# Kernel tuning notes

Hardware: AMD Instinct MI355X
Metric: run time of the kernel (lower is better)

## Reference

```python
import jax, jax.numpy as jnp
from jax import lax
import numpy as np

EPS = 1e-6
B, CIN, HW = 16, 12, 40
E, DEPTH, NH = 768, 12, 12
K, PAD = 10, 5
S = (HW + 2 * PAD - K) // 1 + 1  # 41 (series_len = s0); s1 also 41
L = S * S
HD = E // NH
MLP = 4 * E


def _ln(x, w, b):
    mu = x.mean(-1, keepdims=True)
    xc = x - mu
    var = (xc * xc).mean(-1, keepdims=True)
    return xc * lax.rsqrt(var + EPS) * w + b


def setup_inputs() -> dict:
    key = jax.random.key(0)
    ks = iter(jax.random.split(key, 24))
    r = lambda shape, s=0.02: jax.random.normal(next(ks), shape, jnp.float32) * s
    inp = {
        'x': jax.random.normal(next(ks), (B, CIN, HW, HW), jnp.float32),
        'conv_w': r((E, CIN, K, K)), 'conv_b': jnp.zeros((E,), jnp.float32),
        'pos_embed': r((1, L, E)),
        'ln1_w': jnp.ones((DEPTH, E), jnp.float32), 'ln1_b': jnp.zeros((DEPTH, E), jnp.float32),
        'qkv_w': r((DEPTH, E, 3 * E)), 'qkv_b': jnp.zeros((DEPTH, 3 * E), jnp.float32),
        'proj_w': r((DEPTH, E, E)), 'proj_b': jnp.zeros((DEPTH, E), jnp.float32),
        'ln2_w': jnp.ones((DEPTH, E), jnp.float32), 'ln2_b': jnp.zeros((DEPTH, E), jnp.float32),
        'fc1_w': r((DEPTH, E, MLP)), 'fc1_b': jnp.zeros((DEPTH, MLP), jnp.float32),
        'fc2_w': r((DEPTH, MLP, E)), 'fc2_b': jnp.zeros((DEPTH, E), jnp.float32),
        'lnf_w': jnp.ones((E,), jnp.float32), 'lnf_b': jnp.zeros((E,), jnp.float32),
        'tconv_w': r((E, 1, K, K)), 'tconv_b': jnp.zeros((1,), jnp.float32),
    }
    return inp


def reference(x, conv_w, conv_b, pos_embed, ln1_w, ln1_b, qkv_w, qkv_b,
              proj_w, proj_b, ln2_w, ln2_b, fc1_w, fc1_b, fc2_w, fc2_b,
              lnf_w, lnf_b, tconv_w, tconv_b):
    scale = HD ** -0.5
    # patch embed: Conv2d -> (B, E, 41, 41) -> flatten -> (B, L, E)
    h = lax.conv_general_dilated(x, conv_w, (1, 1), [(PAD, PAD), (PAD, PAD)])
    h = h + conv_b[None, :, None, None]
    t = h.reshape(B, E, L).transpose(0, 2, 1) + pos_embed

    for i in range(DEPTH):
        # attention over each of the S series slices (N = S tokens each), batched
        y = _ln(t, ln1_w[i], ln1_b[i])
        qkv = (y @ qkv_w[i] + qkv_b[i]).reshape(B, S, S, 3, NH, HD)
        q, k, v = qkv[:, :, :, 0], qkv[:, :, :, 1], qkv[:, :, :, 2]  # (B,S,N,NH,HD)
        attn = jnp.einsum('bsnhd,bsmhd->bshnm', q, k) * scale
        attn = jax.nn.softmax(attn, axis=-1)
        o = jnp.einsum('bshnm,bsmhd->bsnhd', attn, v).reshape(B, L, E)
        t = t + (o @ proj_w[i] + proj_b[i])
        # MLP
        z = _ln(t, ln2_w[i], ln2_b[i])
        z = jax.nn.gelu(z @ fc1_w[i] + fc1_b[i], approximate=False)
        t = t + (z @ fc2_w[i] + fc2_b[i])

    t = _ln(t, lnf_w, lnf_b)
    feat = t.reshape(B, S, S, E).transpose(0, 3, 1, 2)  # (B, E, 41, 41)
    # ConvTranspose2d(k=10, s=1, p=5) == direct conv with flipped/swapped kernel, pad k-1-p=4
    wt = jnp.flip(tconv_w, (2, 3)).transpose(1, 0, 2, 3)  # (out_c, E, K, K)
    out = lax.conv_general_dilated(feat, wt, (1, 1), [(K - 1 - PAD,) * 2] * 2)
    out = out + tconv_b[None, :, None, None]
    return jnp.squeeze(out)  # (B, 40, 40)
```

## Files before the change

kernel.cpp:

```cpp
#include <hip/hip_runtime.h>
#include <cstdint>

typedef __bf16 bf16_t;
typedef __attribute__((ext_vector_type(8))) __bf16 bf16x8;
typedef __attribute__((ext_vector_type(4))) __bf16 bf16x4;
typedef __attribute__((ext_vector_type(4))) float f32x4;

#define TOKENS 26896
#define LLEN   1681
#define SDIM   41
#define EDIM   768

__device__ __forceinline__ void gload_lds16(const bf16_t* g, bf16_t* l) {
  auto gp = reinterpret_cast<const __attribute__((address_space(1))) char*>(
      reinterpret_cast<uintptr_t>(g));
  auto lp = reinterpret_cast<__attribute__((address_space(3))) char*>(
      reinterpret_cast<uintptr_t>(l));
  __builtin_amdgcn_global_load_lds(gp, lp, 16, 0, 0);
}

enum { EPI_T_POS = 0, EPI_BF16 = 1, EPI_ADD_T = 2, EPI_GELU = 3, EPI_F32 = 4 };

template <int EPI>
__global__ __launch_bounds__(256, 4) void gemm4_kernel(
    const bf16_t* __restrict__ A, const bf16_t* __restrict__ Bt,
    const float* __restrict__ bias, float* __restrict__ fout,
    bf16_t* __restrict__ bout, const float* __restrict__ pos,
    int M, int N, int K, int ntn, int nwg)
{
  __shared__ bf16_t lds[16384];
  const int tid = threadIdx.x, wave = tid >> 6, lane = tid & 63;
  const int wr = wave >> 1, wc = wave & 1;

  int id = blockIdx.x;
  {
    const int q = nwg >> 3, r = nwg & 7;
    const int xcd = id & 7, ix = id >> 3;
    id = (xcd < r ? xcd * (q + 1) : r * (q + 1) + (xcd - r) * q) + ix;
  }
  const int row0 = (id / ntn) * 128;
  const int col0 = (id % ntn) * 128;
  const int NT = K >> 5;

  const int srow = tid >> 2;
  const int sswz = ((tid & 3) ^ ((srow >> 1) & 3)) * 8;
  const bf16_t* aptr[2];
  const bf16_t* bptr[2];
  #pragma unroll
  for (int p = 0; p < 2; ++p) {
    int ar = row0 + p * 64 + srow; if (ar > M - 1) ar = M - 1;
    int br = col0 + p * 64 + srow; if (br > N - 1) br = N - 1;
    aptr[p] = A  + (size_t)ar * K + sswz;
    bptr[p] = Bt + (size_t)br * K + sswz;
  }
  bf16_t* sdst = lds + tid * 8;

  #define STAGE(BUF, KT) do {                                   \
    const int koff_ = (KT) << 5;                                \
    gload_lds16(aptr[0] + koff_, sdst + (BUF)*8192);            \
    gload_lds16(aptr[1] + koff_, sdst + (BUF)*8192 + 2048);     \
    gload_lds16(bptr[0] + koff_, sdst + (BUF)*8192 + 4096);     \
    gload_lds16(bptr[1] + koff_, sdst + (BUF)*8192 + 6144);     \
  } while (0)

  const int l15 = lane & 15, l4 = lane >> 4;
  const int fswz = (l4 ^ ((l15 >> 1) & 3)) << 3;
  const bf16_t* lA = lds + (wr * 64 + l15) * 32 + fswz;
  const bf16_t* lB = lds + 4096 + (wc * 64 + l15) * 32 + fswz;

  f32x4 acc[4][4] = {};

  #define COMPUTE(BUF) do {                                     \
    bf16x8 fa[4], fb[4];                                        \
    _Pragma("unroll")                                           \
    for (int m_ = 0; m_ < 4; ++m_) fa[m_] = *(const bf16x8*)(lA + (BUF)*8192 + m_*512); \
    _Pragma("unroll")                                           \
    for (int n_ = 0; n_ < 4; ++n_) fb[n_] = *(const bf16x8*)(lB + (BUF)*8192 + n_*512); \
    _Pragma("unroll")                                           \
    for (int m_ = 0; m_ < 4; ++m_)                              \
      _Pragma("unroll")                                         \
      for (int n_ = 0; n_ < 4; ++n_)                            \
        acc[m_][n_] = __builtin_amdgcn_mfma_f32_16x16x32_bf16(fa[m_], fb[n_], acc[m_][n_], 0, 0, 0); \
  } while (0)

  STAGE(0, 0);
  __syncthreads();
  int kt = 0;
  while (kt + 2 <= NT) {
    if (kt + 1 < NT) STAGE(1, kt + 1);
    COMPUTE(0);
    __syncthreads();
    if (kt + 2 < NT) STAGE(0, kt + 2);
    COMPUTE(1);
    __syncthreads();
    kt += 2;
  }
  if (kt < NT) COMPUTE(0);
  #undef STAGE
  #undef COMPUTE

  const int rgrp = lane >> 4;
  #pragma unroll
  for (int m = 0; m < 4; ++m) {
    #pragma unroll
    for (int n = 0; n < 4; ++n) {
      const int col = col0 + wc * 64 + n * 16 + l15;
      if (col >= N) continue;
      const int rbase = row0 + wr * 64 + m * 16 + rgrp * 4;
      float bv = 0.f;
      if constexpr (EPI != EPI_F32) bv = bias[col];
      #pragma unroll
      for (int r = 0; r < 4; ++r) {
        const int rr = rbase + r;
        if (rr >= M) continue;
        const float v = acc[m][n][r] + bv;
        const size_t o = (size_t)rr * N + col;
        if constexpr (EPI == EPI_T_POS) {
          const int l = rr % LLEN;
          fout[o] = v + pos[(size_t)l * N + col];
        } else if constexpr (EPI == EPI_BF16) {
          bout[o] = (bf16_t)v;
        } else if constexpr (EPI == EPI_ADD_T) {
          fout[o] += v;
        } else if constexpr (EPI == EPI_GELU) {
          const float gg = 0.5f * v * (1.f + erff(v * 0.70710678118654752f));
          bout[o] = (bf16_t)gg;
        } else {
          fout[o] = v;
        }
      }
    }
  }
}

__global__ __launch_bounds__(256) void gemm128_f32(
    const bf16_t* __restrict__ A, const bf16_t* __restrict__ Bt,
    float* __restrict__ fout, int M, int N, int K)
{
  __shared__ bf16_t As[128 * 32];
  __shared__ bf16_t Bs[128 * 32];
  const int tid = threadIdx.x, wave = tid >> 6, lane = tid & 63;
  const int row0 = blockIdx.x * 128, col0 = blockIdx.y * 128;
  const int wr = wave >> 1, wc = wave & 1;
  f32x4 acc[4][4] = {};
  const int srow = lane >> 2, skoff = (lane & 3) * 8;
  const int nsteps = K >> 5;
  for (int kt = 0; kt < nsteps; ++kt) {
    const int k0 = kt << 5;
    #pragma unroll
    for (int i = 0; i < 2; ++i) {
      const int r = (i * 4 + wave) * 16 + srow;
      int arow = row0 + r; if (arow > M - 1) arow = M - 1;
      int brow = col0 + r; if (brow > N - 1) brow = N - 1;
      gload_lds16(A  + (size_t)arow * K + k0 + skoff, &As[r * 32 + skoff]);
      gload_lds16(Bt + (size_t)brow * K + k0 + skoff, &Bs[r * 32 + skoff]);
    }
    asm volatile("s_waitcnt vmcnt(0)" ::: "memory");
    __syncthreads();
    const int lrow = lane & 15, lk = (lane >> 4) * 8;
    bf16x8 af[4], bfr[4];
    #pragma unroll
    for (int mi = 0; mi < 4; ++mi)
      af[mi] = *(const bf16x8*)&As[(wr * 64 + mi * 16 + lrow) * 32 + lk];
    #pragma unroll
    for (int ni = 0; ni < 4; ++ni)
      bfr[ni] = *(const bf16x8*)&Bs[(wc * 64 + ni * 16 + lrow) * 32 + lk];
    #pragma unroll
    for (int mi = 0; mi < 4; ++mi)
      #pragma unroll
      for (int ni = 0; ni < 4; ++ni)
        acc[mi][ni] = __builtin_amdgcn_mfma_f32_16x16x32_bf16(af[mi], bfr[ni], acc[mi][ni], 0, 0, 0);
    __syncthreads();
  }
  const int lcol = lane & 15, rgrp = lane >> 4;
  #pragma unroll
  for (int mi = 0; mi < 4; ++mi)
    #pragma unroll
    for (int ni = 0; ni < 4; ++ni) {
      const int col = col0 + wc * 64 + ni * 16 + lcol;
      if (col >= N) continue;
      const int rbase = row0 + wr * 64 + mi * 16 + rgrp * 4;
      #pragma unroll
      for (int r = 0; r < 4; ++r) {
        const int rr = rbase + r;
        if (rr >= M) continue;
        fout[(size_t)rr * N + col] = acc[mi][ni][r];
      }
    }
}

__global__ __launch_bounds__(256) void ln_kernel(
    const float* __restrict__ t, const float* __restrict__ w,
    const float* __restrict__ b, bf16_t* __restrict__ y)
{
  const int token = blockIdx.x * 4 + (threadIdx.x >> 6);
  const int lane  = threadIdx.x & 63;
  const float4* xp = (const float4*)(t + (size_t)token * EDIM);
  float4 v[3];
  float s = 0.f;
  #pragma unroll
  for (int i = 0; i < 3; ++i) {
    v[i] = xp[i * 64 + lane];
    s += v[i].x + v[i].y + v[i].z + v[i].w;
  }
  #pragma unroll
  for (int off = 32; off; off >>= 1) s += __shfl_xor(s, off);
  const float mu = s * (1.f / 768.f);
  float q = 0.f;
  #pragma unroll
  for (int i = 0; i < 3; ++i) {
    const float dx = v[i].x - mu, dy = v[i].y - mu;
    const float dz = v[i].z - mu, dw = v[i].w - mu;
    q += dx * dx + dy * dy + dz * dz + dw * dw;
  }
  #pragma unroll
  for (int off = 32; off; off >>= 1) q += __shfl_xor(q, off);
  const float rs = rsqrtf(q * (1.f / 768.f) + 1e-6f);
  bf16_t* yp = y + (size_t)token * EDIM;
  #pragma unroll
  for (int i = 0; i < 3; ++i) {
    const int e = i * 64 + lane;
    const float4 wv = ((const float4*)w)[e];
    const float4 bv = ((const float4*)b)[e];
    bf16x4 o;
    o[0] = (bf16_t)((v[i].x - mu) * rs * wv.x + bv.x);
    o[1] = (bf16_t)((v[i].y - mu) * rs * wv.y + bv.y);
    o[2] = (bf16_t)((v[i].z - mu) * rs * wv.z + bv.z);
    o[3] = (bf16_t)((v[i].w - mu) * rs * wv.w + bv.w);
    *(bf16x4*)(yp + e * 4) = o;
  }
}

__global__ __launch_bounds__(256) void attn_kernel(
    const bf16_t* __restrict__ qkv, bf16_t* __restrict__ o)
{
  const int blk = blockIdx.x;
  const int h  = blk % 12;
  const int bs = blk / 12;
  const int s1 = bs % SDIM;
  const int b  = bs / SDIM;
  __shared__ float Qs[SDIM][65], Ks[SDIM][65], Vs[SDIM][65], Ps[SDIM][44];
  const int tid = threadIdx.x;
  const size_t base = ((size_t)b * LLEN + (size_t)s1 * SDIM);

  for (int idx = tid; idx < SDIM * 8; idx += 256) {
    const int m = idx >> 3, c = idx & 7;
    const bf16_t* p = qkv + (base + m) * 2304 + h * 64 + c * 8;
    const bf16x8 qv = *(const bf16x8*)(p);
    const bf16x8 kv = *(const bf16x8*)(p + 768);
    const bf16x8 vv = *(const bf16x8*)(p + 1536);
    #pragma unroll
    for (int j = 0; j < 8; ++j) {
      Qs[m][c * 8 + j] = (float)qv[j];
      Ks[m][c * 8 + j] = (float)kv[j];
      Vs[m][c * 8 + j] = (float)vv[j];
    }
  }
  __syncthreads();

  for (int idx = tid; idx < SDIM * SDIM; idx += 256) {
    const int n = idx / SDIM, m = idx % SDIM;
    float s = 0.f;
    #pragma unroll
    for (int d = 0; d < 64; ++d) s += Qs[n][d] * Ks[m][d];
    Ps[n][m] = s * 0.125f;
  }
  __syncthreads();

  {
    const int row = tid >> 2, sub = tid & 3;
    if (row < SDIM) {
      float mx = -1e30f;
      for (int m = sub; m < SDIM; m += 4) mx = fmaxf(mx, Ps[row][m]);
      mx = fmaxf(mx, __shfl_xor(mx, 1));
      mx = fmaxf(mx, __shfl_xor(mx, 2));
      float sum = 0.f;
      for (int m = sub; m < SDIM; m += 4) {
        const float e = __expf(Ps[row][m] - mx);
        Ps[row][m] = e;
        sum += e;
      }
      sum += __shfl_xor(sum, 1);
      sum += __shfl_xor(sum, 2);
      const float inv = 1.f / sum;
      for (int m = sub; m < SDIM; m += 4) Ps[row][m] *= inv;
    }
  }
  __syncthreads();

  for (int idx = tid; idx < SDIM * 64; idx += 256) {
    const int n = idx >> 6, d = idx & 63;
    float s = 0.f;
    #pragma unroll
    for (int m = 0; m < SDIM; ++m) s += Ps[n][m] * Vs[m][d];
    o[(base + n) * EDIM + h * 64 + d] = (bf16_t)s;
  }
}

__global__ __launch_bounds__(256) void transpose_kernel(
    const float* __restrict__ in, bf16_t* __restrict__ out, int K, int N)
{
  __shared__ float tile[32][33];
  const int k0 = blockIdx.x * 32, n0 = blockIdx.y * 32;
  const int tx = threadIdx.x & 31, ty = threadIdx.x >> 5;
  #pragma unroll
  for (int i = 0; i < 32; i += 8) {
    const int k = k0 + ty + i, n = n0 + tx;
    if (k < K && n < N) tile[ty + i][tx] = in[(size_t)k * N + n];
  }
  __syncthreads();
  #pragma unroll
  for (int i = 0; i < 32; i += 8) {
    const int n = n0 + ty + i, k = k0 + tx;
    if (n < N && k < K) out[(size_t)n * K + k] = (bf16_t)tile[tx][ty + i];
  }
}

__global__ __launch_bounds__(256) void im2col_kernel(
    const float* __restrict__ x, bf16_t* __restrict__ col, int tok0, int ntok)
{
  const size_t idx = (size_t)blockIdx.x * 256 + threadIdx.x;
  if (idx >= (size_t)ntok * 1216) return;
  const int kk = (int)(idx % 1216);
  const size_t tok = tok0 + idx / 1216;
  const int b = (int)(tok / LLEN), l = (int)(tok % LLEN);
  const int s1 = l / SDIM, s2 = l % SDIM;
  float v = 0.f;
  if (kk < 1200) {
    const int cin = kk / 100, r = kk % 100, ky = r / 10, kx = r % 10;
    const int iy = s1 - 5 + ky, ix = s2 - 5 + kx;
    if (iy >= 0 && iy < 40 && ix >= 0 && ix < 40)
      v = x[((size_t)(b * 12 + cin) * 40 + iy) * 40 + ix];
  }
  col[idx] = (bf16_t)v;
}

__global__ __launch_bounds__(256) void convw_kernel(
    const float* __restrict__ w, bf16_t* __restrict__ out)
{
  const int idx = blockIdx.x * 256 + threadIdx.x;
  const int kk = idx % 1216, e = idx / 1216;
  const float v = (kk < 1200) ? w[(size_t)e * 1200 + kk] : 0.f;
  out[idx] = (bf16_t)v;
}

__global__ __launch_bounds__(256) void tconvw_kernel(
    const float* __restrict__ w, bf16_t* __restrict__ out)
{
  const int idx = blockIdx.x * 256 + threadIdx.x;
  const int e = idx % 768, tap = idx / 768;
  const int ky = tap / 10, kx = tap % 10;
  out[idx] = (bf16_t)w[(size_t)e * 100 + (9 - ky) * 10 + (9 - kx)];
}

__global__ __launch_bounds__(256) void outconv_kernel(
    const float* __restrict__ g, const float* __restrict__ tb,
    float* __restrict__ out)
{
  const int idx = blockIdx.x * 256 + threadIdx.x;
  if (idx >= 16 * 40 * 40) return;
  const int x = idx % 40, y = (idx / 40) % 40, b = idx / 1600;
  float s = tb[0];
  #pragma unroll
  for (int ky = 0; ky < 10; ++ky) {
    const int ty_ = y - 4 + ky;
    if (ty_ < 0 || ty_ >= SDIM) continue;
    #pragma unroll
    for (int kx = 0; kx < 10; ++kx) {
      const int tx_ = x - 4 + kx;
      if (tx_ < 0 || tx_ >= SDIM) continue;
      s += g[((size_t)b * LLEN + ty_ * SDIM + tx_) * 100 + ky * 10 + kx];
    }
  }
  out[idx] = s;
}

extern "C" void kernel_launch(void* const* d_in, const int* in_sizes, int n_in,
                              void* d_out, int out_size, void* d_ws, size_t ws_size,
                              hipStream_t stream)
{
  const float* x       = (const float*)d_in[0];
  const float* conv_w  = (const float*)d_in[1];
  const float* conv_b  = (const float*)d_in[2];
  const float* pos     = (const float*)d_in[3];
  const float* ln1_w   = (const float*)d_in[4];
  const float* ln1_b   = (const float*)d_in[5];
  const float* qkv_w   = (const float*)d_in[6];
  const float* qkv_b   = (const float*)d_in[7];
  const float* proj_w  = (const float*)d_in[8];
  const float* proj_b  = (const float*)d_in[9];
  const float* ln2_w   = (const float*)d_in[10];
  const float* ln2_b   = (const float*)d_in[11];
  const float* fc1_w   = (const float*)d_in[12];
  const float* fc1_b   = (const float*)d_in[13];
  const float* fc2_w   = (const float*)d_in[14];
  const float* fc2_b   = (const float*)d_in[15];
  const float* lnf_w   = (const float*)d_in[16];
  const float* lnf_b   = (const float*)d_in[17];
  const float* tconv_w = (const float*)d_in[18];
  const float* tconv_b = (const float*)d_in[19];
  float* out = (float*)d_out;

  const int nch = (ws_size >= 303500000UL) ? 1
                : (ws_size >= 220900000UL) ? 2 : 4;
  const int cht = TOKENS / nch;

  char* p = (char*)d_ws;
  auto alloc = [&](size_t bytes) {
    char* r = p;
    p += (bytes + 255) & ~(size_t)255;
    return r;
  };
  bf16_t* wbuf = (bf16_t*)alloc((size_t)768 * 9216 * 2);
  float*  t    = (float*)alloc((size_t)TOKENS * EDIM * 4);
  bf16_t* ybuf = (bf16_t*)alloc((size_t)TOKENS * EDIM * 2);
  bf16_t* hbuf = (bf16_t*)alloc((size_t)cht * 3072 * 2);

  bf16_t* Wq = wbuf;
  bf16_t* Wp = Wq + (size_t)2304 * 768;
  bf16_t* W1 = Wp + (size_t)768 * 768;
  bf16_t* W2 = W1 + (size_t)3072 * 768;

  auto g4 = [&](int epi, const bf16_t* A, const bf16_t* Bt,
                const float* bias, float* fo, bf16_t* bo, const float* pe,
                int M, int N, int K) {
    const int mtiles = (M + 127) / 128;
    const int ntn = N / 128;
    const int nwg = mtiles * ntn;
    switch (epi) {
      case EPI_T_POS: gemm4_kernel<EPI_T_POS><<<nwg, 256, 0, stream>>>(A, Bt, bias, fo, bo, pe, M, N, K, ntn, nwg); break;
      case EPI_BF16:  gemm4_kernel<EPI_BF16 ><<<nwg, 256, 0, stream>>>(A, Bt, bias, fo, bo, pe, M, N, K, ntn, nwg); break;
      case EPI_ADD_T: gemm4_kernel<EPI_ADD_T><<<nwg, 256, 0, stream>>>(A, Bt, bias, fo, bo, pe, M, N, K, ntn, nwg); break;
      default:        gemm4_kernel<EPI_GELU ><<<nwg, 256, 0, stream>>>(A, Bt, bias, fo, bo, pe, M, N, K, ntn, nwg); break;
    }
  };

  convw_kernel<<<(768 * 1216) / 256, 256, 0, stream>>>(conv_w, wbuf);
  for (int c = 0; c < nch; ++c) {
    const int tok0 = c * cht;
    im2col_kernel<<<(unsigned)(((size_t)cht * 1216 + 255) / 256), 256, 0, stream>>>(x, hbuf, tok0, cht);
    g4(EPI_T_POS, hbuf, wbuf, conv_b, t + (size_t)tok0 * EDIM, nullptr, pos, cht, EDIM, 1216);
  }

  for (int i = 0; i < 12; ++i) {
    transpose_kernel<<<dim3(24, 72), 256, 0, stream>>>(qkv_w + (size_t)i * 768 * 2304, Wq, 768, 2304);
    transpose_kernel<<<dim3(24, 24), 256, 0, stream>>>(proj_w + (size_t)i * 768 * 768, Wp, 768, 768);
    transpose_kernel<<<dim3(24, 96), 256, 0, stream>>>(fc1_w + (size_t)i * 768 * 3072, W1, 768, 3072);
    transpose_kernel<<<dim3(96, 24), 256, 0, stream>>>(fc2_w + (size_t)i * 3072 * 768, W2, 3072, 768);

    ln_kernel<<<TOKENS / 4, 256, 0, stream>>>(t, ln1_w + i * EDIM, ln1_b + i * EDIM, ybuf);
    for (int c = 0; c < nch; ++c) {
      const size_t ro = (size_t)c * cht;
      g4(EPI_BF16, ybuf + ro * EDIM, Wq, qkv_b + i * 2304, nullptr, hbuf, nullptr, cht, 2304, 768);
      attn_kernel<<<(16 / nch) * SDIM * 12, 256, 0, stream>>>(hbuf, ybuf + ro * EDIM);
    }
    g4(EPI_ADD_T, ybuf, Wp, proj_b + i * EDIM, t, nullptr, nullptr, TOKENS, EDIM, 768);

    ln_kernel<<<TOKENS / 4, 256, 0, stream>>>(t, ln2_w + i * EDIM, ln2_b + i * EDIM, ybuf);
    for (int c = 0; c < nch; ++c) {
      const size_t ro = (size_t)c * cht;
      g4(EPI_GELU, ybuf + ro * EDIM, W1, fc1_b + i * 3072, nullptr, hbuf, nullptr, cht, 3072, 768);
      g4(EPI_ADD_T, hbuf, W2, fc2_b + i * EDIM, t + ro * EDIM, nullptr, nullptr, cht, EDIM, 3072);
    }
  }

  ln_kernel<<<TOKENS / 4, 256, 0, stream>>>(t, lnf_w, lnf_b, ybuf);
  tconvw_kernel<<<(100 * 768) / 256, 256, 0, stream>>>(tconv_w, wbuf);
  gemm128_f32<<<dim3((TOKENS + 127) / 128, 1), 256, 0, stream>>>(ybuf, wbuf, (float*)hbuf, TOKENS, 100, 768);
  outconv_kernel<<<100, 256, 0, stream>>>((const float*)hbuf, tconv_b, out);
}
```

Before: 10.94 ms.

## Store residual stream in bf16 instead of fp32

Switches the residual activation buffer t from fp32 to bf16. The GEMM epilogues now write or accumulate in bf16, and the LayerNorm kernel reads bf16 with wider vector loads. This halves residual read/write traffic in the LN and residual-add GEMMs and shrinks the workspace, which lowers the thresholds for using fewer token chunks. The cost is accuracy: 24 residual additions rounded to bf16 may accumulate error beyond tolerance.

Result: faster. 10.20 ms (-6.7%).

```diff
diff --git a/kernel.cpp b/kernel.cpp
--- a/kernel.cpp
+++ b/kernel.cpp
@@ -117,11 +117,11 @@
         const size_t o = (size_t)rr * N + col;
         if constexpr (EPI == EPI_T_POS) {
           const int l = rr % LLEN;
-          fout[o] = v + pos[(size_t)l * N + col];
+          bout[o] = (bf16_t)(v + pos[(size_t)l * N + col]);
         } else if constexpr (EPI == EPI_BF16) {
           bout[o] = (bf16_t)v;
         } else if constexpr (EPI == EPI_ADD_T) {
-          fout[o] += v;
+          bout[o] = (bf16_t)((float)bout[o] + v);
         } else if constexpr (EPI == EPI_GELU) {
           const float gg = 0.5f * v * (1.f + erff(v * 0.70710678118654752f));
           bout[o] = (bf16_t)gg;
@@ -190,44 +190,60 @@
 }
 
 __global__ __launch_bounds__(256) void ln_kernel(
-    const float* __restrict__ t, const float* __restrict__ w,
+    const bf16_t* __restrict__ t, const float* __restrict__ w,
     const float* __restrict__ b, bf16_t* __restrict__ y)
 {
   const int token = blockIdx.x * 4 + (threadIdx.x >> 6);
   const int lane  = threadIdx.x & 63;
-  const float4* xp = (const float4*)(t + (size_t)token * EDIM);
-  float4 v[3];
+  const bf16_t* xp = t + (size_t)token * EDIM;
+  const bf16x8 a8 = *(const bf16x8*)(xp + lane * 8);
+  const bf16x4 a4 = *(const bf16x4*)(xp + 512 + lane * 4);
+  float va[12];
+  #pragma unroll
+  for (int j = 0; j < 8; ++j) va[j] = (float)a8[j];
+  #pragma unroll
+  for (int j = 0; j < 4; ++j) va[8 + j] = (float)a4[j];
   float s = 0.f;
   #pragma unroll
-  for (int i = 0; i < 3; ++i) {
-    v[i] = xp[i * 64 + lane];
-    s += v[i].x + v[i].y + v[i].z + v[i].w;
-  }
+  for (int j = 0; j < 12; ++j) s += va[j];
   #pragma unroll
   for (int off = 32; off; off >>= 1) s += __shfl_xor(s, off);
   const float mu = s * (1.f / 768.f);
   float q = 0.f;
   #pragma unroll
-  for (int i = 0; i < 3; ++i) {
-    const float dx = v[i].x - mu, dy = v[i].y - mu;
-    const float dz = v[i].z - mu, dw = v[i].w - mu;
-    q += dx * dx + dy * dy + dz * dz + dw * dw;
-  }
+  for (int j = 0; j < 12; ++j) { const float d = va[j] - mu; q += d * d; }
   #pragma unroll
   for (int off = 32; off; off >>= 1) q += __shfl_xor(q, off);
   const float rs = rsqrtf(q * (1.f / 768.f) + 1e-6f);
+
   bf16_t* yp = y + (size_t)token * EDIM;
-  #pragma unroll
-  for (int i = 0; i < 3; ++i) {
-    const int e = i * 64 + lane;
-    const float4 wv = ((const float4*)w)[e];
-    const float4 bv = ((const float4*)b)[e];
+  {
+    const int e0 = lane * 8;
+    const float4 w0 = ((const float4*)(w + e0))[0];
+    const float4 w1 = ((const float4*)(w + e0))[1];
+    const float4 b0 = ((const float4*)(b + e0))[0];
+    const float4 b1 = ((const float4*)(b + e0))[1];
+    bf16x8 o;
+    o[0] = (bf16_t)((va[0] - mu) * rs * w0.x + b0.x);
+    o[1] = (bf16_t)((va[1] - mu) * rs * w0.y + b0.y);
+    o[2] = (bf16_t)((va[2] - mu) * rs * w0.z + b0.z);
+    o[3] = (bf16_t)((va[3] - mu) * rs * w0.w + b0.w);
+    o[4] = (bf16_t)((va[4] - mu) * rs * w1.x + b1.x);
+    o[5] = (bf16_t)((va[5] - mu) * rs * w1.y + b1.y);
+    o[6] = (bf16_t)((va[6] - mu) * rs * w1.z + b1.z);
+    o[7] = (bf16_t)((va[7] - mu) * rs * w1.w + b1.w);
+    *(bf16x8*)(yp + e0) = o;
+  }
+  {
+    const int e0 = 512 + lane * 4;
+    const float4 w0 = *(const float4*)(w + e0);
+    const float4 b0 = *(const float4*)(b + e0);
     bf16x4 o;
-    o[0] = (bf16_t)((v[i].x - mu) * rs * wv.x + bv.x);
-    o[1] = (bf16_t)((v[i].y - mu) * rs * wv.y + bv.y);
-    o[2] = (bf16_t)((v[i].z - mu) * rs * wv.z + bv.z);
-    o[3] = (bf16_t)((v[i].w - mu) * rs * wv.w + bv.w);
-    *(bf16x4*)(yp + e * 4) = o;
+    o[0] = (bf16_t)((va[8]  - mu) * rs * w0.x + b0.x);
+    o[1] = (bf16_t)((va[9]  - mu) * rs * w0.y + b0.y);
+    o[2] = (bf16_t)((va[10] - mu) * rs * w0.z + b0.z);
+    o[3] = (bf16_t)((va[11] - mu) * rs * w0.w + b0.w);
+    *(bf16x4*)(yp + e0) = o;
   }
 }
 
@@ -401,8 +417,8 @@
   const float* tconv_b = (const float*)d_in[19];
   float* out = (float*)d_out;
 
-  const int nch = (ws_size >= 303500000UL) ? 1
-                : (ws_size >= 220900000UL) ? 2 : 4;
+  const int nch = (ws_size >= 262200000UL) ? 1
+                : (ws_size >= 179500000UL) ? 2 : 4;
   const int cht = TOKENS / nch;
 
   char* p = (char*)d_ws;
@@ -412,7 +428,7 @@
     return r;
   };
   bf16_t* wbuf = (bf16_t*)alloc((size_t)768 * 9216 * 2);
-  float*  t    = (float*)alloc((size_t)TOKENS * EDIM * 4);
+  bf16_t* t    = (bf16_t*)alloc((size_t)TOKENS * EDIM * 2);
   bf16_t* ybuf = (bf16_t*)alloc((size_t)TOKENS * EDIM * 2);
   bf16_t* hbuf = (bf16_t*)alloc((size_t)cht * 3072 * 2);
 
@@ -422,16 +438,16 @@
   bf16_t* W2 = W1 + (size_t)3072 * 768;
 
   auto g4 = [&](int epi, const bf16_t* A, const bf16_t* Bt,
-                const float* bias, float* fo, bf16_t* bo, const float* pe,
+                const float* bias, bf16_t* bo, const float* pe,
                 int M, int N, int K) {
     const int mtiles = (M + 127) / 128;
     const int ntn = N / 128;
     const int nwg = mtiles * ntn;
     switch (epi) {
-      case EPI_T_POS: gemm4_kernel<EPI_T_POS><<<nwg, 256, 0, stream>>>(A, Bt, bias, fo, bo, pe, M, N, K, ntn, nwg); break;
-      case EPI_BF16:  gemm4_kernel<EPI_BF16 ><<<nwg, 256, 0, stream>>>(A, Bt, bias, fo, bo, pe, M, N, K, ntn, nwg); break;
-      case EPI_ADD_T: gemm4_kernel<EPI_ADD_T><<<nwg, 256, 0, stream>>>(A, Bt, bias, fo, bo, pe, M, N, K, ntn, nwg); break;
-      default:        gemm4_kernel<EPI_GELU ><<<nwg, 256, 0, stream>>>(A, Bt, bias, fo, bo, pe, M, N, K, ntn, nwg); break;
+      case EPI_T_POS: gemm4_kernel<EPI_T_POS><<<nwg, 256, 0, stream>>>(A, Bt, bias, nullptr, bo, pe, M, N, K, ntn, nwg); break;
+      case EPI_BF16:  gemm4_kernel<EPI_BF16 ><<<nwg, 256, 0, stream>>>(A, Bt, bias, nullptr, bo, pe, M, N, K, ntn, nwg); break;
+      case EPI_ADD_T: gemm4_kernel<EPI_ADD_T><<<nwg, 256, 0, stream>>>(A, Bt, bias, nullptr, bo, pe, M, N, K, ntn, nwg); break;
+      default:        gemm4_kernel<EPI_GELU ><<<nwg, 256, 0, stream>>>(A, Bt, bias, nullptr, bo, pe, M, N, K, ntn, nwg); break;
     }
   };
 
@@ -439,7 +455,7 @@
   for (int c = 0; c < nch; ++c) {
     const int tok0 = c * cht;
     im2col_kernel<<<(unsigned)(((size_t)cht * 1216 + 255) / 256), 256, 0, stream>>>(x, hbuf, tok0, cht);
-    g4(EPI_T_POS, hbuf, wbuf, conv_b, t + (size_t)tok0 * EDIM, nullptr, pos, cht, EDIM, 1216);
+    g4(EPI_T_POS, hbuf, wbuf, conv_b, t + (size_t)tok0 * EDIM, pos, cht, EDIM, 1216);
   }
 
   for (int i = 0; i < 12; ++i) {
@@ -451,16 +467,16 @@
     ln_kernel<<<TOKENS / 4, 256, 0, stream>>>(t, ln1_w + i * EDIM, ln1_b + i * EDIM, ybuf);
     for (int c = 0; c < nch; ++c) {
       const size_t ro = (size_t)c * cht;
-      g4(EPI_BF16, ybuf + ro * EDIM, Wq, qkv_b + i * 2304, nullptr, hbuf, nullptr, cht, 2304, 768);
+      g4(EPI_BF16, ybuf + ro * EDIM, Wq, qkv_b + i * 2304, hbuf, nullptr, cht, 2304, 768);
       attn_kernel<<<(16 / nch) * SDIM * 12, 256, 0, stream>>>(hbuf, ybuf + ro * EDIM);
     }
-    g4(EPI_ADD_T, ybuf, Wp, proj_b + i * EDIM, t, nullptr, nullptr, TOKENS, EDIM, 768);
+    g4(EPI_ADD_T, ybuf, Wp, proj_b + i * EDIM, t, nullptr, TOKENS, EDIM, 768);
 
     ln_kernel<<<TOKENS / 4, 256, 0, stream>>>(t, ln2_w + i * EDIM, ln2_b + i * EDIM, ybuf);
     for (int c = 0; c < nch; ++c) {
       const size_t ro = (size_t)c * cht;
-      g4(EPI_GELU, ybuf + ro * EDIM, W1, fc1_b + i * 3072, nullptr, hbuf, nullptr, cht, 3072, 768);
-      g4(EPI_ADD_T, hbuf, W2, fc2_b + i * EDIM, t + ro * EDIM, nullptr, nullptr, cht, EDIM, 3072);
+      g4(EPI_GELU, ybuf + ro * EDIM, W1, fc1_b + i * 3072, hbuf, nullptr, cht, 3072, 768);
+      g4(EPI_ADD_T, hbuf, W2, fc2_b + i * EDIM, t + ro * EDIM, nullptr, cht, EDIM, 3072);
     }
   }
 
```
